# Optimization experiments

Measured on AMD Instinct MI355X. Metric: run time of the kernel, lower is better.

## Reference

```python
import jax, jax.numpy as jnp
import numpy as np

N = 4096      # num_nodes
DIN = 16      # num_inputs
C = 16        # comm_channels
CHQ = 8       # ch_q
K = 10        # value-iteration steps
GAMMA = 0.99
EPS = float(np.finfo(np.float32).eps)


def setup_inputs() -> dict:
    key = jax.random.key(0)
    ks = jax.random.split(key, 8)
    x = jax.random.normal(ks[0], (N, DIN), dtype=jnp.float32)
    comms = jnp.zeros((N, C), dtype=jnp.float32)  # fresh comm state (reset())
    # random symmetric 0/1 adjacency, ~20 avg degree, zero diagonal
    u = jax.random.uniform(ks[1], (N, N), dtype=jnp.float32)
    a = (u < 0.005).astype(jnp.float32)
    adj = jnp.maximum(a, a.T) * (1.0 - jnp.eye(N, dtype=jnp.float32))
    mask = jnp.ones((N,), dtype=jnp.float32)
    # parameters (torch Linear: y = x @ W + b, weights stored [in, out] here)
    Wr = jax.random.normal(ks[2], (DIN + C, 1), dtype=jnp.float32) * 0.1   # reward_encoding
    br = jnp.zeros((1,), dtype=jnp.float32)
    We = jax.random.normal(ks[3], (DIN + C, CHQ), dtype=jnp.float32) * 0.1  # encoder
    be = jnp.zeros((CHQ,), dtype=jnp.float32)
    w_emb = jax.random.normal(ks[4], (CHQ,), dtype=jnp.float32) * 0.1       # embedder (ch_q -> 1)
    b_emb = jnp.zeros((), dtype=jnp.float32)
    Wa = jax.random.normal(ks[5], (CHQ,), dtype=jnp.float32) * 0.1          # action_decoding (1 -> ch_q)
    ba = jnp.zeros((CHQ,), dtype=jnp.float32)
    return dict(x=x, comms=comms, adj=adj, mask=mask, Wr=Wr, br=br,
                We=We, be=be, w_emb=w_emb, b_emb=b_emb, Wa=Wa, ba=ba, k=K)


def reference(x, comms, adj, mask, Wr, br, We, be, w_emb, b_emb, Wa, ba, k):
    n = adj.shape[0]
    # initialize_adj: symmetric normalization D^{-1/2} (A + I) D^{-1/2}
    a_norm = adj + jnp.eye(n, dtype=adj.dtype)
    deg = a_norm.sum(axis=0)
    dinv_sqrt = jnp.sqrt(1.0 / (deg + EPS))
    k3 = a_norm * dinv_sqrt[:, None] * dinv_sqrt[None, :]

    xc = jnp.concatenate([x, comms], axis=1)          # [n, DIN+C]
    r = (xc @ Wr + br)[:, 0]                          # reward per node [n]
    # embedder(cols - rows) fused: score[i,j] = s[j] - s[i] + b_emb
    s = (xc @ We + be) @ w_emb                        # [n]
    kernel3 = k3 * (s[None, :] - s[:, None] + b_emb)  # [n, n]

    # k-step value iteration
    v = jnp.zeros_like(r)
    for _ in range(k):
        k3v = kernel3 @ (r + GAMMA * v)               # [n]
        q = k3v[:, None] * Wa[None, :] + ba           # action_decoding (1 -> ch_q): [n, ch_q]
        v = q.max(axis=-1)                            # [n]

    # final_feature_process (rl=False): additive -inf mask
    return v + jnp.where(mask == 0, -jnp.inf, 0.0)
```

## Files before the change

### kernel.cpp

```cpp
#include <hip/hip_runtime.h>
#include <math.h>

#define NN     4096
#define NB     256
#define TPB    1024
#define WPB    16
#define CAP    128
#define SLOT   80
#define NB2    32
#define NPB2   128
#define MAXE   10
#define CSRW   (NPB2 * SLOT)
#define GAMMA  0.99f
#define EPSF   1.1920929e-07f
#define KSTEPS 10


__device__ __forceinline__ unsigned long long pk2(float lo, float hi) {
    return ((unsigned long long)__float_as_uint(hi) << 32) |
            (unsigned long long)__float_as_uint(lo);
}
__device__ __forceinline__ float lo_f(unsigned long long z) {
    return __uint_as_float((unsigned int)z);
}
__device__ __forceinline__ float hi_f(unsigned long long z) {
    return __uint_as_float((unsigned int)(z >> 32));
}
__device__ __forceinline__ unsigned long long pkVT(float v, int tag) {
    return ((unsigned long long)(unsigned int)tag << 32) |
            (unsigned long long)__float_as_uint(v);
}
__device__ __forceinline__ int tag_of(unsigned long long z) {
    return (int)(unsigned int)(z >> 32);
}

__global__ void __launch_bounds__(TPB) gvin_nobar(
    const float* __restrict__ adj,  const float* __restrict__ x,
    const float* __restrict__ comms,const float* __restrict__ mask,
    const float* __restrict__ Wr,   const float* __restrict__ br,
    const float* __restrict__ We,   const float* __restrict__ be,
    const float* __restrict__ w_emb,const float* __restrict__ b_emb,
    const float* __restrict__ Wa,   const float* __restrict__ ba,
    unsigned long long* PD, unsigned long long* SS,
    unsigned long long* UT0, unsigned long long* UT1, int* CNT, int* CSRG,
    float* __restrict__ out)
{
    __shared__ int nbr[WPB][CAP];
    __shared__ int lcnt[WPB];
    __shared__ unsigned long long PDL[NN];
    __shared__ float UL[NN];
    __shared__ int   CSRL[CSRW];
    __shared__ int   CNTL[NPB2];
    __shared__ float SSL[NPB2];
    const int tid  = (int)threadIdx.x;
    const int wave = tid >> 6;
    const int lane = tid & 63;
    const int g = (int)blockIdx.x * WPB + wave;

    if (lane == 0) { lcnt[wave] = 1; nbr[wave][0] = g; }

    const float4* rowp = (const float4*)(adj + (size_t)g * NN);
#pragma unroll 4
    for (int it = 0; it < 16; ++it) {
        const float4 v = rowp[lane + it * 64];
        const int b4 = (lane + it * 64) * 4;
        if (v.x != 0.0f) { int sl = atomicAdd(&lcnt[wave], 1); if (sl < CAP) nbr[wave][sl] = b4;     }
        if (v.y != 0.0f) { int sl = atomicAdd(&lcnt[wave], 1); if (sl < CAP) nbr[wave][sl] = b4 + 1; }
        if (v.z != 0.0f) { int sl = atomicAdd(&lcnt[wave], 1); if (sl < CAP) nbr[wave][sl] = b4 + 2; }
        if (v.w != 0.0f) { int sl = atomicAdd(&lcnt[wave], 1); if (sl < CAP) nbr[wave][sl] = b4 + 3; }
    }

    float pr = 0.0f, ps = 0.0f;
    if (lane < 32) {
        const float xc = (lane < 16) ? x[g * 16 + lane] : comms[g * 16 + (lane - 16)];
        float we = 0.0f;
#pragma unroll
        for (int c = 0; c < 8; ++c) we += We[lane * 8 + c] * w_emb[c];
        pr = xc * Wr[lane];
        ps = xc * we;
    } else if (lane == 32) {
#pragma unroll
        for (int c = 0; c < 8; ++c) ps += be[c] * w_emb[c];
        pr = br[0];
    }
#pragma unroll
    for (int off = 32; off; off >>= 1) { pr += __shfl_xor(pr, off); ps += __shfl_xor(ps, off); }
    const float r = pr, s = ps;

    const int   deg  = lcnt[wave];
    const int   cl   = deg < CAP ? deg : CAP;
    const int   clp  = cl < SLOT ? cl : SLOT;
    const float dinv = sqrtf(1.0f / ((float)deg + EPSF));
    const float p    = dinv * (s + b_emb[0]);

    if (lane == 0) {
        __hip_atomic_store(PD  + g, pk2(p, dinv), __ATOMIC_RELAXED, __HIP_MEMORY_SCOPE_AGENT);
        __hip_atomic_store(SS  + g, pkVT(s, 0),   __ATOMIC_RELAXED, __HIP_MEMORY_SCOPE_AGENT);
        __hip_atomic_store(UT0 + g, pkVT(r, 0),   __ATOMIC_RELAXED, __HIP_MEMORY_SCOPE_AGENT);
        __hip_atomic_store(CNT + g, clp,          __ATOMIC_RELAXED, __HIP_MEMORY_SCOPE_AGENT);
    }
    if (lane < clp)
        __hip_atomic_store(CSRG + g * SLOT + lane, nbr[wave][lane],
                           __ATOMIC_RELAXED, __HIP_MEMORY_SCOPE_AGENT);
    if (64 + lane < clp)
        __hip_atomic_store(CSRG + g * SLOT + 64 + lane, nbr[wave][64 + lane],
                           __ATOMIC_RELAXED, __HIP_MEMORY_SCOPE_AGENT);

    if (blockIdx.x >= NB2) return;

    const int base = (int)blockIdx.x * NPB2;

    if (tid < NPB2) {
        int c;
        while ((c = __hip_atomic_load(CNT + base + tid, __ATOMIC_RELAXED,
                                      __HIP_MEMORY_SCOPE_AGENT)) < 1)
            __builtin_amdgcn_s_sleep(2);
        CNTL[tid] = c;
        unsigned long long z;
        for (;;) {
            z = __hip_atomic_load(SS + base + tid, __ATOMIC_RELAXED,
                                  __HIP_MEMORY_SCOPE_AGENT);
            if (tag_of(z) == 0) break;
            __builtin_amdgcn_s_sleep(2);
        }
        SSL[tid] = lo_f(z);
    }
    __syncthreads();

    {
        const int* gcsr = CSRG + (size_t)base * SLOT;
#pragma unroll
        for (int i = 0; i < MAXE; ++i) {
            const int idx = tid + (i << 10);
            const int nq  = idx / SLOT;
            const int k   = idx - nq * SLOT;
            if (k < CNTL[nq]) {
                int vj;
                while ((vj = __hip_atomic_load(gcsr + idx, __ATOMIC_RELAXED,
                                               __HIP_MEMORY_SCOPE_AGENT)) < 0)
                    __builtin_amdgcn_s_sleep(2);
                CSRL[idx] = vj;
            }
        }
    }

    {
        unsigned long long z0, z1, z2, z3;
        for (;;) {
            asm volatile(
                "global_load_dwordx2 %0, %4, off sc1\n\t"
                "global_load_dwordx2 %1, %5, off sc1\n\t"
                "global_load_dwordx2 %2, %6, off sc1\n\t"
                "global_load_dwordx2 %3, %7, off sc1\n\t"
                "s_waitcnt vmcnt(0)"
                : "=&v"(z0), "=&v"(z1), "=&v"(z2), "=&v"(z3)
                : "v"(PD + tid), "v"(PD + tid + 1024),
                  "v"(PD + tid + 2048), "v"(PD + tid + 3072)
                : "memory");
            const bool ok = (hi_f(z0) > 0.0f) && (hi_f(z1) > 0.0f) &&
                            (hi_f(z2) > 0.0f) && (hi_f(z3) > 0.0f);
            if (__all(ok)) break;
            __builtin_amdgcn_s_sleep(2);
        }
        PDL[tid] = z0; PDL[tid + 1024] = z1;
        PDL[tid + 2048] = z2; PDL[tid + 3072] = z3;
    }
    __syncthreads();

    const int q   = tid >> 3, sub = tid & 7;
    const int n   = base + q;
    const int dgn = CNTL[q];
    int jj[MAXE]; float pe[MAXE], de[MAXE];
#pragma unroll
    for (int e = 0; e < MAXE; ++e) {
        const int k  = sub + (e << 3);
        const bool vv = k < dgn;
        jj[e] = vv ? CSRL[q * SLOT + k] : 0;
        const unsigned long long z = PDL[jj[e]];
        pe[e] = vv ? lo_f(z) : 0.0f;
        de[e] = vv ? hi_f(z) : 0.0f;
    }
    float rn = 0.0f, sn = 0.0f, dvn = 0.0f;
    if (sub == 0) { sn = SSL[q]; dvn = hi_f(PDL[n]); }
    float wa[8], bb[8];
#pragma unroll
    for (int c = 0; c < 8; ++c) { wa[c] = Wa[c]; bb[c] = ba[c]; }

    const int widx = (wave << 8) + lane;
    const unsigned long long* __restrict__ UTbase[2] = { UT0, UT1 };

    float v = 0.0f;
    for (int t = 0; t < KSTEPS; ++t) {
        const unsigned long long* Uin  = UTbase[t & 1];
        unsigned long long*       Uout = (unsigned long long*)UTbase[(t + 1) & 1];

        unsigned long long z0, z1, z2, z3;
        for (;;) {
            asm volatile(
                "global_load_dwordx2 %0, %4, off sc1\n\t"
                "global_load_dwordx2 %1, %5, off sc1\n\t"
                "global_load_dwordx2 %2, %6, off sc1\n\t"
                "global_load_dwordx2 %3, %7, off sc1\n\t"
                "s_waitcnt vmcnt(0)"
                : "=&v"(z0), "=&v"(z1), "=&v"(z2), "=&v"(z3)
                : "v"(Uin + widx), "v"(Uin + widx + 64),
                  "v"(Uin + widx + 128), "v"(Uin + widx + 192)
                : "memory");
            const bool ok = (tag_of(z0) == t) && (tag_of(z1) == t) &&
                            (tag_of(z2) == t) && (tag_of(z3) == t);
            if (__all(ok)) break;
            __builtin_amdgcn_s_sleep(2);
        }
        UL[widx]       = lo_f(z0);
        UL[widx + 64]  = lo_f(z1);
        UL[widx + 128] = lo_f(z2);
        UL[widx + 192] = lo_f(z3);
        __syncthreads();

        if (t == 0 && sub == 0) rn = UL[n];

        float a1 = 0.0f, a2 = 0.0f;
#pragma unroll
        for (int e = 0; e < MAXE; ++e) {
            const float u = UL[jj[e]];
            a1 = fmaf(pe[e], u, a1);
            a2 = fmaf(de[e], u, a2);
        }
        a1 += __shfl_xor(a1, 1); a2 += __shfl_xor(a2, 1);
        a1 += __shfl_xor(a1, 2); a2 += __shfl_xor(a2, 2);
        a1 += __shfl_xor(a1, 4); a2 += __shfl_xor(a2, 4);

        if (sub == 0) {
            const float k3v = dvn * (a1 - sn * a2);
            v = fmaf(k3v, wa[0], bb[0]);
#pragma unroll
            for (int c = 1; c < 8; ++c) v = fmaxf(v, fmaf(k3v, wa[c], bb[c]));
            if (t < KSTEPS - 1)
                __hip_atomic_store(Uout + n, pkVT(rn + GAMMA * v, t + 1),
                                   __ATOMIC_RELAXED, __HIP_MEMORY_SCOPE_AGENT);
        }
        if (t < KSTEPS - 1)
            __syncthreads();
    }

    if (sub == 0) out[n] = v + (mask[n] == 0.0f ? -INFINITY : 0.0f);
}

extern "C" void kernel_launch(void* const* d_in, const int* in_sizes, int n_in,
                              void* d_out, int out_size, void* d_ws, size_t ws_size,
                              hipStream_t stream) {
    const float* x     = (const float*)d_in[0];
    const float* comms = (const float*)d_in[1];
    const float* adj   = (const float*)d_in[2];
    const float* mask  = (const float*)d_in[3];
    const float* Wr    = (const float*)d_in[4];
    const float* br    = (const float*)d_in[5];
    const float* We    = (const float*)d_in[6];
    const float* be    = (const float*)d_in[7];
    const float* w_emb = (const float*)d_in[8];
    const float* b_emb = (const float*)d_in[9];
    const float* Wa    = (const float*)d_in[10];
    const float* ba    = (const float*)d_in[11];

    char* ws = (char*)d_ws;
    size_t off = 0;
    unsigned long long* PD  = (unsigned long long*)(ws + off); off += (size_t)NN * 8;
    unsigned long long* SS  = (unsigned long long*)(ws + off); off += (size_t)NN * 8;
    unsigned long long* UT0 = (unsigned long long*)(ws + off); off += (size_t)NN * 8;
    unsigned long long* UT1 = (unsigned long long*)(ws + off); off += (size_t)NN * 8;
    int* CNT                = (int*)(ws + off); off += (size_t)NN * 4;
    int* CSRG               = (int*)(ws + off); off += (size_t)NN * SLOT * 4;
    float* out = (float*)d_out;

    gvin_nobar<<<dim3(NB), dim3(TPB), 0, stream>>>(
        adj, x, comms, mask, Wr, br, We, be, w_emb, b_emb, Wa, ba,
        PD, SS, UT0, UT1, CNT, CSRG, out);
}
```

Baseline: 149.4 us.

## Halve value-iteration blocks, drop CSR staging, and poll only unready chunks

The value-iteration phase now runs on 16 blocks of 256 nodes each instead of 32 blocks of 128. Each node is handled by 4 lanes with up to 20 edges per lane, down from 8 lanes with up to 10, so the shuffle reduction loses one step. Neighbour indices are read straight from the global CSR into registers, removing the shared-memory CSR stage and one block barrier. The spin-wait loops now re-poll only the 64-lane chunks that are not yet ready. The goal is less inter-block flag traffic and synchronisation per step, at the cost of more serial edge work per lane and fewer blocks doing the gather.

```diff
diff --git a/kernel.cpp b/kernel.cpp
--- a/kernel.cpp
+++ b/kernel.cpp
@@ -7,10 +7,10 @@
 #define WPB    16
 #define CAP    128
 #define SLOT   80
-#define NB2    32
-#define NPB2   128
-#define MAXE   10
-#define CSRW   (NPB2 * SLOT)
+#define NB2    16
+#define NPB2   256
+#define SUBS   4
+#define MAXE   20
 #define GAMMA  0.99f
 #define EPSF   1.1920929e-07f
 #define KSTEPS 10
@@ -34,7 +34,7 @@
     return (int)(unsigned int)(z >> 32);
 }
 
-__global__ void __launch_bounds__(TPB) gvin_nobar(
+__global__ void __launch_bounds__(TPB) gvin_nb16(
     const float* __restrict__ adj,  const float* __restrict__ x,
     const float* __restrict__ comms,const float* __restrict__ mask,
     const float* __restrict__ Wr,   const float* __restrict__ br,
@@ -49,7 +49,6 @@
     __shared__ int lcnt[WPB];
     __shared__ unsigned long long PDL[NN];
     __shared__ float UL[NN];
-    __shared__ int   CSRL[CSRW];
     __shared__ int   CNTL[NPB2];
     __shared__ float SSL[NPB2];
     const int tid  = (int)threadIdx.x;
@@ -125,57 +124,56 @@
         }
         SSL[tid] = lo_f(z);
     }
-    __syncthreads();
-
-    {
-        const int* gcsr = CSRG + (size_t)base * SLOT;
-#pragma unroll
-        for (int i = 0; i < MAXE; ++i) {
-            const int idx = tid + (i << 10);
-            const int nq  = idx / SLOT;
-            const int k   = idx - nq * SLOT;
-            if (k < CNTL[nq]) {
-                int vj;
-                while ((vj = __hip_atomic_load(gcsr + idx, __ATOMIC_RELAXED,
-                                               __HIP_MEMORY_SCOPE_AGENT)) < 0)
-                    __builtin_amdgcn_s_sleep(2);
-                CSRL[idx] = vj;
-            }
-        }
-    }
 
     {
         unsigned long long z0, z1, z2, z3;
-        for (;;) {
-            asm volatile(
-                "global_load_dwordx2 %0, %4, off sc1\n\t"
-                "global_load_dwordx2 %1, %5, off sc1\n\t"
-                "global_load_dwordx2 %2, %6, off sc1\n\t"
-                "global_load_dwordx2 %3, %7, off sc1\n\t"
-                "s_waitcnt vmcnt(0)"
-                : "=&v"(z0), "=&v"(z1), "=&v"(z2), "=&v"(z3)
-                : "v"(PD + tid), "v"(PD + tid + 1024),
-                  "v"(PD + tid + 2048), "v"(PD + tid + 3072)
-                : "memory");
-            const bool ok = (hi_f(z0) > 0.0f) && (hi_f(z1) > 0.0f) &&
-                            (hi_f(z2) > 0.0f) && (hi_f(z3) > 0.0f);
-            if (__all(ok)) break;
-            __builtin_amdgcn_s_sleep(2);
+        asm volatile(
+            "global_load_dwordx2 %0, %4, off sc1\n\t"
+            "global_load_dwordx2 %1, %5, off sc1\n\t"
+            "global_load_dwordx2 %2, %6, off sc1\n\t"
+            "global_load_dwordx2 %3, %7, off sc1\n\t"
+            "s_waitcnt vmcnt(0)"
+            : "=&v"(z0), "=&v"(z1), "=&v"(z2), "=&v"(z3)
+            : "v"(PD + tid), "v"(PD + tid + 1024),
+              "v"(PD + tid + 2048), "v"(PD + tid + 3072)
+            : "memory");
+        bool k0 = __all(hi_f(z0) > 0.0f), k1 = __all(hi_f(z1) > 0.0f);
+        bool k2 = __all(hi_f(z2) > 0.0f), k3 = __all(hi_f(z3) > 0.0f);
+        while (!(k0 && k1 && k2 && k3)) {
+            __builtin_amdgcn_s_sleep(2);
+            if (!k0) { asm volatile("global_load_dwordx2 %0, %1, off sc1\n\ts_waitcnt vmcnt(0)"
+                                    : "=v"(z0) : "v"(PD + tid) : "memory");
+                       k0 = __all(hi_f(z0) > 0.0f); }
+            if (!k1) { asm volatile("global_load_dwordx2 %0, %1, off sc1\n\ts_waitcnt vmcnt(0)"
+                                    : "=v"(z1) : "v"(PD + tid + 1024) : "memory");
+                       k1 = __all(hi_f(z1) > 0.0f); }
+            if (!k2) { asm volatile("global_load_dwordx2 %0, %1, off sc1\n\ts_waitcnt vmcnt(0)"
+                                    : "=v"(z2) : "v"(PD + tid + 2048) : "memory");
+                       k2 = __all(hi_f(z2) > 0.0f); }
+            if (!k3) { asm volatile("global_load_dwordx2 %0, %1, off sc1\n\ts_waitcnt vmcnt(0)"
+                                    : "=v"(z3) : "v"(PD + tid + 3072) : "memory");
+                       k3 = __all(hi_f(z3) > 0.0f); }
         }
         PDL[tid] = z0; PDL[tid + 1024] = z1;
         PDL[tid + 2048] = z2; PDL[tid + 3072] = z3;
     }
     __syncthreads();
 
-    const int q   = tid >> 3, sub = tid & 7;
+    const int q   = tid >> 2, sub = tid & 3;
     const int n   = base + q;
     const int dgn = CNTL[q];
     int jj[MAXE]; float pe[MAXE], de[MAXE];
 #pragma unroll
     for (int e = 0; e < MAXE; ++e) {
-        const int k  = sub + (e << 3);
+        const int k  = sub + (e << 2);
         const bool vv = k < dgn;
-        jj[e] = vv ? CSRL[q * SLOT + k] : 0;
+        int vj = 0;
+        if (vv) {
+            while ((vj = __hip_atomic_load(CSRG + n * SLOT + k, __ATOMIC_RELAXED,
+                                           __HIP_MEMORY_SCOPE_AGENT)) < 0)
+                __builtin_amdgcn_s_sleep(2);
+        }
+        jj[e] = vv ? vj : 0;
         const unsigned long long z = PDL[jj[e]];
         pe[e] = vv ? lo_f(z) : 0.0f;
         de[e] = vv ? hi_f(z) : 0.0f;
@@ -187,29 +185,39 @@
     for (int c = 0; c < 8; ++c) { wa[c] = Wa[c]; bb[c] = ba[c]; }
 
     const int widx = (wave << 8) + lane;
-    const unsigned long long* __restrict__ UTbase[2] = { UT0, UT1 };
 
     float v = 0.0f;
     for (int t = 0; t < KSTEPS; ++t) {
-        const unsigned long long* Uin  = UTbase[t & 1];
-        unsigned long long*       Uout = (unsigned long long*)UTbase[(t + 1) & 1];
+        const unsigned long long* Uin  = (t & 1) ? UT1 : UT0;
+        unsigned long long*       Uout = (t & 1) ? UT0 : UT1;
 
         unsigned long long z0, z1, z2, z3;
-        for (;;) {
-            asm volatile(
-                "global_load_dwordx2 %0, %4, off sc1\n\t"
-                "global_load_dwordx2 %1, %5, off sc1\n\t"
-                "global_load_dwordx2 %2, %6, off sc1\n\t"
-                "global_load_dwordx2 %3, %7, off sc1\n\t"
-                "s_waitcnt vmcnt(0)"
-                : "=&v"(z0), "=&v"(z1), "=&v"(z2), "=&v"(z3)
-                : "v"(Uin + widx), "v"(Uin + widx + 64),
-                  "v"(Uin + widx + 128), "v"(Uin + widx + 192)
-                : "memory");
-            const bool ok = (tag_of(z0) == t) && (tag_of(z1) == t) &&
-                            (tag_of(z2) == t) && (tag_of(z3) == t);
-            if (__all(ok)) break;
-            __builtin_amdgcn_s_sleep(2);
+        asm volatile(
+            "global_load_dwordx2 %0, %4, off sc1\n\t"
+            "global_load_dwordx2 %1, %5, off sc1\n\t"
+            "global_load_dwordx2 %2, %6, off sc1\n\t"
+            "global_load_dwordx2 %3, %7, off sc1\n\t"
+            "s_waitcnt vmcnt(0)"
+            : "=&v"(z0), "=&v"(z1), "=&v"(z2), "=&v"(z3)
+            : "v"(Uin + widx), "v"(Uin + widx + 64),
+              "v"(Uin + widx + 128), "v"(Uin + widx + 192)
+            : "memory");
+        bool k0 = __all(tag_of(z0) == t), k1 = __all(tag_of(z1) == t);
+        bool k2 = __all(tag_of(z2) == t), k3 = __all(tag_of(z3) == t);
+        while (!(k0 && k1 && k2 && k3)) {
+            __builtin_amdgcn_s_sleep(2);
+            if (!k0) { asm volatile("global_load_dwordx2 %0, %1, off sc1\n\ts_waitcnt vmcnt(0)"
+                                    : "=v"(z0) : "v"(Uin + widx) : "memory");
+                       k0 = __all(tag_of(z0) == t); }
+            if (!k1) { asm volatile("global_load_dwordx2 %0, %1, off sc1\n\ts_waitcnt vmcnt(0)"
+                                    : "=v"(z1) : "v"(Uin + widx + 64) : "memory");
+                       k1 = __all(tag_of(z1) == t); }
+            if (!k2) { asm volatile("global_load_dwordx2 %0, %1, off sc1\n\ts_waitcnt vmcnt(0)"
+                                    : "=v"(z2) : "v"(Uin + widx + 128) : "memory");
+                       k2 = __all(tag_of(z2) == t); }
+            if (!k3) { asm volatile("global_load_dwordx2 %0, %1, off sc1\n\ts_waitcnt vmcnt(0)"
+                                    : "=v"(z3) : "v"(Uin + widx + 192) : "memory");
+                       k3 = __all(tag_of(z3) == t); }
         }
         UL[widx]       = lo_f(z0);
         UL[widx + 64]  = lo_f(z1);
@@ -228,7 +236,6 @@
         }
         a1 += __shfl_xor(a1, 1); a2 += __shfl_xor(a2, 1);
         a1 += __shfl_xor(a1, 2); a2 += __shfl_xor(a2, 2);
-        a1 += __shfl_xor(a1, 4); a2 += __shfl_xor(a2, 4);
 
         if (sub == 0) {
             const float k3v = dvn * (a1 - sn * a2);
@@ -272,7 +279,7 @@
     int* CSRG               = (int*)(ws + off); off += (size_t)NN * SLOT * 4;
     float* out = (float*)d_out;
 
-    gvin_nobar<<<dim3(NB), dim3(TPB), 0, stream>>>(
+    gvin_nb16<<<dim3(NB), dim3(TPB), 0, stream>>>(
         adj, x, comms, mask, Wr, br, We, be, w_emb, b_emb, Wa, ba,
         PD, SS, UT0, UT1, CNT, CSRG, out);
 }
```

New measurement: 153.8 us. 2.9% more time.

## Run value-iteration phase on a single XCD with L2-scoped flag polling

Applied to the files above, without the earlier changes.

The value-iteration blocks are now chosen dynamically: only blocks running on XCC 0 claim one of 32 slots through an atomic counter, so all cross-block exchanges stay within one XCD's L2. Per-step loads and stores of the tagged value table then use sc0 (L2-coherent) instead of sc1 system-level accesses, and polling retries only the chunks that are not ready yet, escalating to sc1 every 16 rounds as a fallback. This is meant to cut the latency of the inter-block handoff in each of the 10 iterations. It adds a memset launch and relies on XCC 0 hosting at least 32 co-resident blocks, otherwise the iteration phase would deadlock.

```diff
diff --git a/kernel.cpp b/kernel.cpp
--- a/kernel.cpp
+++ b/kernel.cpp
@@ -34,7 +34,14 @@
     return (int)(unsigned int)(z >> 32);
 }
 
-__global__ void __launch_bounds__(TPB) gvin_nobar(
+#define LD2_SC0(dst, addr)                                                  \
+    asm volatile("global_load_dwordx2 %0, %1, off sc0\n\ts_waitcnt vmcnt(0)" \
+                 : "=v"(dst) : "v"(addr) : "memory")
+#define LD2_SC1(dst, addr)                                                  \
+    asm volatile("global_load_dwordx2 %0, %1, off sc1\n\ts_waitcnt vmcnt(0)" \
+                 : "=v"(dst) : "v"(addr) : "memory")
+
+__global__ void __launch_bounds__(TPB) gvin_xcd(
     const float* __restrict__ adj,  const float* __restrict__ x,
     const float* __restrict__ comms,const float* __restrict__ mask,
     const float* __restrict__ Wr,   const float* __restrict__ br,
@@ -43,7 +50,7 @@
     const float* __restrict__ Wa,   const float* __restrict__ ba,
     unsigned long long* PD, unsigned long long* SS,
     unsigned long long* UT0, unsigned long long* UT1, int* CNT, int* CSRG,
-    float* __restrict__ out)
+    int* CLM, float* __restrict__ out)
 {
     __shared__ int nbr[WPB][CAP];
     __shared__ int lcnt[WPB];
@@ -52,6 +59,7 @@
     __shared__ int   CSRL[CSRW];
     __shared__ int   CNTL[NPB2];
     __shared__ float SSL[NPB2];
+    __shared__ int   slotL;
     const int tid  = (int)threadIdx.x;
     const int wave = tid >> 6;
     const int lane = tid & 63;
@@ -106,9 +114,15 @@
         __hip_atomic_store(CSRG + g * SLOT + 64 + lane, nbr[wave][64 + lane],
                            __ATOMIC_RELAXED, __HIP_MEMORY_SCOPE_AGENT);
 
-    if (blockIdx.x >= NB2) return;
-
-    const int base = (int)blockIdx.x * NPB2;
+    int xcc;
+    asm volatile("s_getreg_b32 %0, hwreg(HW_REG_XCC_ID, 0, 4)" : "=s"(xcc));
+    if (xcc != 0) return;
+    if (tid == 0) slotL = atomicAdd(CLM, 1);
+    __syncthreads();
+    const int slot = slotL;
+    if (slot >= NB2) return;
+
+    const int base = slot * NPB2;
 
     if (tid < NPB2) {
         int c;
@@ -187,15 +201,14 @@
     for (int c = 0; c < 8; ++c) { wa[c] = Wa[c]; bb[c] = ba[c]; }
 
     const int widx = (wave << 8) + lane;
-    const unsigned long long* __restrict__ UTbase[2] = { UT0, UT1 };
 
     float v = 0.0f;
     for (int t = 0; t < KSTEPS; ++t) {
-        const unsigned long long* Uin  = UTbase[t & 1];
-        unsigned long long*       Uout = (unsigned long long*)UTbase[(t + 1) & 1];
+        const unsigned long long* Uin  = (t & 1) ? UT1 : UT0;
+        unsigned long long*       Uout = (t & 1) ? UT0 : UT1;
 
         unsigned long long z0, z1, z2, z3;
-        for (;;) {
+        if (t == 0) {
             asm volatile(
                 "global_load_dwordx2 %0, %4, off sc1\n\t"
                 "global_load_dwordx2 %1, %5, off sc1\n\t"
@@ -206,10 +219,32 @@
                 : "v"(Uin + widx), "v"(Uin + widx + 64),
                   "v"(Uin + widx + 128), "v"(Uin + widx + 192)
                 : "memory");
-            const bool ok = (tag_of(z0) == t) && (tag_of(z1) == t) &&
-                            (tag_of(z2) == t) && (tag_of(z3) == t);
-            if (__all(ok)) break;
+        } else {
+            asm volatile(
+                "global_load_dwordx2 %0, %4, off sc0\n\t"
+                "global_load_dwordx2 %1, %5, off sc0\n\t"
+                "global_load_dwordx2 %2, %6, off sc0\n\t"
+                "global_load_dwordx2 %3, %7, off sc0\n\t"
+                "s_waitcnt vmcnt(0)"
+                : "=&v"(z0), "=&v"(z1), "=&v"(z2), "=&v"(z3)
+                : "v"(Uin + widx), "v"(Uin + widx + 64),
+                  "v"(Uin + widx + 128), "v"(Uin + widx + 192)
+                : "memory");
+        }
+        bool k0 = __all(tag_of(z0) == t), k1 = __all(tag_of(z1) == t);
+        bool k2 = __all(tag_of(z2) == t), k3 = __all(tag_of(z3) == t);
+        int rounds = 0;
+        while (!(k0 && k1 && k2 && k3)) {
             __builtin_amdgcn_s_sleep(2);
+            const bool esc = (t == 0) || ((++rounds & 15) == 0);
+            if (!k0) { if (esc) LD2_SC1(z0, Uin + widx);       else LD2_SC0(z0, Uin + widx);
+                       k0 = __all(tag_of(z0) == t); }
+            if (!k1) { if (esc) LD2_SC1(z1, Uin + widx + 64);  else LD2_SC0(z1, Uin + widx + 64);
+                       k1 = __all(tag_of(z1) == t); }
+            if (!k2) { if (esc) LD2_SC1(z2, Uin + widx + 128); else LD2_SC0(z2, Uin + widx + 128);
+                       k2 = __all(tag_of(z2) == t); }
+            if (!k3) { if (esc) LD2_SC1(z3, Uin + widx + 192); else LD2_SC0(z3, Uin + widx + 192);
+                       k3 = __all(tag_of(z3) == t); }
         }
         UL[widx]       = lo_f(z0);
         UL[widx + 64]  = lo_f(z1);
@@ -235,9 +270,11 @@
             v = fmaf(k3v, wa[0], bb[0]);
 #pragma unroll
             for (int c = 1; c < 8; ++c) v = fmaxf(v, fmaf(k3v, wa[c], bb[c]));
-            if (t < KSTEPS - 1)
-                __hip_atomic_store(Uout + n, pkVT(rn + GAMMA * v, t + 1),
-                                   __ATOMIC_RELAXED, __HIP_MEMORY_SCOPE_AGENT);
+            if (t < KSTEPS - 1) {
+                const unsigned long long w = pkVT(rn + GAMMA * v, t + 1);
+                asm volatile("global_store_dwordx2 %0, %1, off sc0"
+                             :: "v"(Uout + n), "v"(w) : "memory");
+            }
         }
         if (t < KSTEPS - 1)
             __syncthreads();
@@ -270,9 +307,12 @@
     unsigned long long* UT1 = (unsigned long long*)(ws + off); off += (size_t)NN * 8;
     int* CNT                = (int*)(ws + off); off += (size_t)NN * 4;
     int* CSRG               = (int*)(ws + off); off += (size_t)NN * SLOT * 4;
+    int* CLM                = (int*)(ws + off); off += 64;
     float* out = (float*)d_out;
 
-    gvin_nobar<<<dim3(NB), dim3(TPB), 0, stream>>>(
+    hipMemsetAsync(CLM, 0, sizeof(int), stream);
+
+    gvin_xcd<<<dim3(NB), dim3(TPB), 0, stream>>>(
         adj, x, comms, mask, Wr, br, We, be, w_emb, b_emb, Wa, ba,
-        PD, SS, UT0, UT1, CNT, CSRG, out);
-}
+        PD, SS, UT0, UT1, CNT, CSRG, CLM, out);
+}
```

New measurement: 202.0 us. 35.2% more time.
